# Kernel optimization log

Hardware: AMD Instinct MI355X
Metric: run time of the kernel (lower is better)

The kernel has to match this reference:

```python
import jax, jax.numpy as jnp
import numpy as np

EPS = 1e-12  # matches torch.nn.functional.normalize default eps


def _normalize(v):
    # L2 normalize along last dim, clamping the norm like torch F.normalize
    n = jnp.linalg.norm(v, axis=-1, keepdims=True)
    return v / jnp.maximum(n, EPS)


def setup_inputs() -> dict:
    key = jax.random.key(0)
    k1, k2 = jax.random.split(key)
    B, K, D, H, W = 64, 5, 1024, 32, 32
    cue = jax.random.normal(k1, (B, K, D), dtype=jnp.float32)
    patches = jax.random.normal(k2, (B, H, W, D), dtype=jnp.float32)
    return {"cue": cue, "patches": patches}


def reference(cue, patches):
    b, k, d = cue.shape
    _, h, w, _ = patches.shape
    cue_n = _normalize(cue)
    patches_n = _normalize(patches)
    flat = patches_n.reshape(b, h * w, d)
    # cosine similarity between each cue and every patch
    sims = jnp.einsum('bkd,bnd->bkn', cue_n, flat)  # (b, k, h*w)
    idx = jnp.argmax(sims, axis=-1)                 # (b, k)
    y = idx // w + 1                                # +1 for pad offset
    x = idx % w + 1
    # zero-pad spatial dims by 1 on each side
    pad = jnp.pad(patches, ((0, 0), (1, 1), (1, 1), (0, 0)))
    offs = jnp.arange(-1, 2)
    yy = y[:, :, None, None] + offs[None, None, :, None]  # (b, k, 3, 1)
    xx = x[:, :, None, None] + offs[None, None, None, :]  # (b, k, 1, 3)
    bidx = jnp.arange(b)[:, None, None, None]
    gathered = pad[bidx, yy, xx, :]                 # (b, k, 3, 3, d)
    roi = gathered.mean(axis=(2, 3))                # (b, k, d)
    return roi
```

## Files before the change

### kernel.cpp

```cpp
#include <hip/hip_runtime.h>
#include <math.h>

#define B 64
#define K 5
#define D 1024
#define H 32
#define W 32
#define N (H * W)

__device__ __forceinline__ float wave_sum(float v) {
#pragma unroll
    for (int off = 32; off > 0; off >>= 1) v += __shfl_down(v, off, 64);
    return v;
}

__device__ __forceinline__ float dot4(float4 a, float4 b) {
    return a.x * b.x + a.y * b.y + a.z * b.z + a.w * b.w;
}

__global__ __launch_bounds__(256) void normalize_cue(const float* __restrict__ cue,
                                                     float* __restrict__ cue_n) {
    const int row = blockIdx.x;
    const int tid = threadIdx.x;
    const float4* src = (const float4*)(cue + (size_t)row * D);
    float4 p = src[tid];
    float ss = p.x * p.x + p.y * p.y + p.z * p.z + p.w * p.w;
    ss = wave_sum(ss);
    __shared__ float smem[4];
    __shared__ float s_inv;
    const int lane = tid & 63, wid = tid >> 6;
    if (lane == 0) smem[wid] = ss;
    __syncthreads();
    if (tid == 0) {
        float t = smem[0] + smem[1] + smem[2] + smem[3];
        s_inv = 1.0f / fmaxf(sqrtf(t), 1e-12f);
    }
    __syncthreads();
    const float inv = s_inv;
    float4 o = make_float4(p.x * inv, p.y * inv, p.z * inv, p.w * inv);
    ((float4*)(cue_n + (size_t)row * D))[tid] = o;
}

__global__ __launch_bounds__(256) void sims_kernel(const float* __restrict__ patches,
                                                   const float* __restrict__ cue_n,
                                                   float* __restrict__ sims) {
    const int wave = threadIdx.x >> 6;
    const int lane = threadIdx.x & 63;
    const int bn0 = blockIdx.x * 8 + wave * 2;
    const int b = bn0 >> 10;
    const int n0 = bn0 & (N - 1);

    const float4* p0 = (const float4*)(patches + (size_t)bn0 * D);
    const float4* p1 = (const float4*)(patches + (size_t)(bn0 + 1) * D);
    const float4* crow = (const float4*)(cue_n + (size_t)b * K * D);

    float na = 0.f, nb = 0.f;
    float da[K], db[K];
#pragma unroll
    for (int k = 0; k < K; ++k) { da[k] = 0.f; db[k] = 0.f; }

#pragma unroll
    for (int j = 0; j < 4; ++j) {
        const int idx = j * 64 + lane;
        float4 pa = p0[idx];
        float4 pb = p1[idx];
        na += dot4(pa, pa);
        nb += dot4(pb, pb);
#pragma unroll
        for (int k = 0; k < K; ++k) {
            float4 c = crow[(size_t)k * (D / 4) + idx];
            da[k] += dot4(pa, c);
            db[k] += dot4(pb, c);
        }
    }

    na = wave_sum(na);
    nb = wave_sum(nb);
#pragma unroll
    for (int k = 0; k < K; ++k) {
        da[k] = wave_sum(da[k]);
        db[k] = wave_sum(db[k]);
    }

    if (lane == 0) {
        const float ia = 1.0f / fmaxf(sqrtf(na), 1e-12f);
        const float ib = 1.0f / fmaxf(sqrtf(nb), 1e-12f);
#pragma unroll
        for (int k = 0; k < K; ++k) {
            sims[((size_t)b * K + k) * N + n0] = da[k] * ia;
            sims[((size_t)b * K + k) * N + n0 + 1] = db[k] * ib;
        }
    }
}

__global__ __launch_bounds__(256) void argmax_gather(const float* __restrict__ sims,
                                                     const float* __restrict__ patches,
                                                     float* __restrict__ out) {
    const int row = blockIdx.x;
    const int b = row / K;
    const int tid = threadIdx.x;

    const float* srow = sims + (size_t)row * N;
    float best = -INFINITY;
    int bidx = 0;
#pragma unroll
    for (int j = 0; j < 4; ++j) {
        const int d = tid * 4 + j;
        const float v = srow[d];
        if (v > best) { best = v; bidx = d; }
    }
#pragma unroll
    for (int off = 32; off > 0; off >>= 1) {
        const float ov = __shfl_down(best, off, 64);
        const int oi = __shfl_down(bidx, off, 64);
        if (ov > best || (ov == best && oi < bidx)) { best = ov; bidx = oi; }
    }
    __shared__ float sv[4];
    __shared__ int si[4];
    __shared__ int s_final;
    const int lane = tid & 63, wid = tid >> 6;
    if (lane == 0) { sv[wid] = best; si[wid] = bidx; }
    __syncthreads();
    if (tid == 0) {
        float bv = sv[0];
        int bi = si[0];
        for (int w2 = 1; w2 < 4; ++w2) {
            if (sv[w2] > bv || (sv[w2] == bv && si[w2] < bi)) { bv = sv[w2]; bi = si[w2]; }
        }
        s_final = bi;
    }
    __syncthreads();

    const int idx = s_final;
    const int y0 = idx >> 5;
    const int x0 = idx & 31;

    float4 acc = make_float4(0.f, 0.f, 0.f, 0.f);
#pragma unroll
    for (int dy = -1; dy <= 1; ++dy) {
        const int yy = y0 + dy;
        if (yy < 0 || yy >= H) continue;
#pragma unroll
        for (int dx = -1; dx <= 1; ++dx) {
            const int xx = x0 + dx;
            if (xx < 0 || xx >= W) continue;
            const float4* nrow =
                (const float4*)(patches + (((size_t)b * H + yy) * W + xx) * D);
            float4 p = nrow[tid];
            acc.x += p.x; acc.y += p.y; acc.z += p.z; acc.w += p.w;
        }
    }
    const float inv9 = 1.0f / 9.0f;
    float4 o = make_float4(acc.x * inv9, acc.y * inv9, acc.z * inv9, acc.w * inv9);
    ((float4*)(out + (size_t)row * D))[tid] = o;
}

extern "C" void kernel_launch(void* const* d_in, const int* in_sizes, int n_in,
                              void* d_out, int out_size, void* d_ws, size_t ws_size,
                              hipStream_t stream) {
    const float* cue = (const float*)d_in[0];
    const float* patches = (const float*)d_in[1];
    float* out = (float*)d_out;

    float* cue_n = (float*)d_ws;
    float* sims = cue_n + (size_t)B * K * D;

    normalize_cue<<<B * K, 256, 0, stream>>>(cue, cue_n);
    sims_kernel<<<(B * N) / 8, 256, 0, stream>>>(patches, cue_n, sims);
    argmax_gather<<<B * K, 256, 0, stream>>>(sims, patches, out);
}
```

Measured before the change: 364.9 us.

## Process four patch rows per wave with butterfly transpose-reduce in sims kernel

Each wave now handles four patch rows instead of two, so every cue vector load is reused across more rows. The 24 per-lane partial sums are reduced with a butterfly shuffle that halves the active values at each step, replacing independent full wave reductions, and the results pass through shared memory so that 20 lanes write the outputs. The argmax kernel also reads each thread's four similarity values as a single float4. The trade-off is higher register pressure and an added block-wide barrier.

```diff
diff --git a/kernel.cpp b/kernel.cpp
--- a/kernel.cpp
+++ b/kernel.cpp
@@ -46,50 +46,69 @@
                                                    float* __restrict__ sims) {
     const int wave = threadIdx.x >> 6;
     const int lane = threadIdx.x & 63;
-    const int bn0 = blockIdx.x * 8 + wave * 2;
+    const int bn0 = blockIdx.x * 16 + wave * 4;
     const int b = bn0 >> 10;
     const int n0 = bn0 & (N - 1);
 
-    const float4* p0 = (const float4*)(patches + (size_t)bn0 * D);
-    const float4* p1 = (const float4*)(patches + (size_t)(bn0 + 1) * D);
+    const float4* prow = (const float4*)(patches + (size_t)bn0 * D);
     const float4* crow = (const float4*)(cue_n + (size_t)b * K * D);
 
-    float na = 0.f, nb = 0.f;
-    float da[K], db[K];
+    float acc[24];
 #pragma unroll
-    for (int k = 0; k < K; ++k) { da[k] = 0.f; db[k] = 0.f; }
+    for (int v = 0; v < 24; ++v) acc[v] = 0.f;
 
 #pragma unroll
     for (int j = 0; j < 4; ++j) {
         const int idx = j * 64 + lane;
-        float4 pa = p0[idx];
-        float4 pb = p1[idx];
-        na += dot4(pa, pa);
-        nb += dot4(pb, pb);
+        float4 p[4];
+#pragma unroll
+        for (int r = 0; r < 4; ++r) p[r] = prow[r * 256 + idx];
+#pragma unroll
+        for (int r = 0; r < 4; ++r) acc[r * 6] += dot4(p[r], p[r]);
 #pragma unroll
         for (int k = 0; k < K; ++k) {
-            float4 c = crow[(size_t)k * (D / 4) + idx];
-            da[k] += dot4(pa, c);
-            db[k] += dot4(pb, c);
+            float4 c = crow[k * 256 + idx];
+#pragma unroll
+            for (int r = 0; r < 4; ++r) acc[r * 6 + 1 + k] += dot4(p[r], c);
         }
     }
 
-    na = wave_sum(na);
-    nb = wave_sum(nb);
 #pragma unroll
-    for (int k = 0; k < K; ++k) {
-        da[k] = wave_sum(da[k]);
-        db[k] = wave_sum(db[k]);
+    for (int i = 0; i < 12; ++i) {
+        float t = (lane & 1) ? acc[i] : acc[i + 12];
+        float r = __shfl_xor(t, 1, 64);
+        acc[i] = ((lane & 1) ? acc[i + 12] : acc[i]) + r;
+    }
+#pragma unroll
+    for (int i = 0; i < 6; ++i) {
+        float t = (lane & 2) ? acc[i] : acc[i + 6];
+        float r = __shfl_xor(t, 2, 64);
+        acc[i] = ((lane & 2) ? acc[i + 6] : acc[i]) + r;
+    }
+#pragma unroll
+    for (int i = 0; i < 3; ++i) {
+        float t = (lane & 4) ? acc[i] : acc[i + 3];
+        float r = __shfl_xor(t, 4, 64);
+        acc[i] = ((lane & 4) ? acc[i + 3] : acc[i]) + r;
+    }
+#pragma unroll
+    for (int m = 8; m <= 32; m <<= 1) {
+#pragma unroll
+        for (int i = 0; i < 3; ++i) acc[i] += __shfl_xor(acc[i], m, 64);
     }
 
-    if (lane == 0) {
-        const float ia = 1.0f / fmaxf(sqrtf(na), 1e-12f);
-        const float ib = 1.0f / fmaxf(sqrtf(nb), 1e-12f);
-#pragma unroll
-        for (int k = 0; k < K; ++k) {
-            sims[((size_t)b * K + k) * N + n0] = da[k] * ia;
-            sims[((size_t)b * K + k) * N + n0 + 1] = db[k] * ib;
-        }
+    __shared__ float slab[4][24];
+    if (lane < 8) {
+        const int base = 12 * (lane & 1) + 6 * ((lane >> 1) & 1) + 3 * ((lane >> 2) & 1);
+        slab[wave][base + 0] = acc[0];
+        slab[wave][base + 1] = acc[1];
+        slab[wave][base + 2] = acc[2];
+    }
+    __syncthreads();
+    if (lane < 4 * K) {
+        const int r = lane / K, k = lane % K;
+        const float inv = 1.0f / fmaxf(sqrtf(slab[wave][r * 6]), 1e-12f);
+        sims[((size_t)b * K + k) * N + n0 + r] = slab[wave][r * 6 + 1 + k] * inv;
     }
 }
 
@@ -100,15 +119,13 @@
     const int b = row / K;
     const int tid = threadIdx.x;
 
-    const float* srow = sims + (size_t)row * N;
-    float best = -INFINITY;
-    int bidx = 0;
-#pragma unroll
-    for (int j = 0; j < 4; ++j) {
-        const int d = tid * 4 + j;
-        const float v = srow[d];
-        if (v > best) { best = v; bidx = d; }
-    }
+    const float4* srow = (const float4*)(sims + (size_t)row * N);
+    float4 v = srow[tid];
+    float best = v.x;
+    int bidx = tid * 4;
+    if (v.y > best) { best = v.y; bidx = tid * 4 + 1; }
+    if (v.z > best) { best = v.z; bidx = tid * 4 + 2; }
+    if (v.w > best) { best = v.w; bidx = tid * 4 + 3; }
 #pragma unroll
     for (int off = 32; off > 0; off >>= 1) {
         const float ov = __shfl_down(best, off, 64);
@@ -166,6 +183,6 @@
     float* sims = cue_n + (size_t)B * K * D;
 
     normalize_cue<<<B * K, 256, 0, stream>>>(cue, cue_n);
-    sims_kernel<<<(B * N) / 8, 256, 0, stream>>>(patches, cue_n, sims);
+    sims_kernel<<<(B * N) / 16, 256, 0, stream>>>(patches, cue_n, sims);
     argmax_gather<<<B * K, 256, 0, stream>>>(sims, patches, out);
 }
```

Result: no change. 362.8 us (-0.6%).
